# Kernel optimization log

Hardware: AMD Instinct MI355X
Metric: run time of the kernel (lower is better)

The kernel has to match this reference:

```python
import jax, jax.numpy as jnp
import numpy as np

N_P, N_A, N_T = 20000, 10000, 5000
D_IN, D_OUT = 512, 256
E_P, E_A, E_T = 320000, 160000, 80000


def setup_inputs() -> dict:
    key = jax.random.key(0)
    ks = iter(jax.random.split(key, 64))

    def nrm(shape, scale=1.0):
        return jax.random.normal(next(ks), shape, dtype=jnp.float32) * scale

    def xav(shape):
        # xavier_uniform-like scale (gain 1.414), normal draw is fine for a baseline
        return nrm(shape, 1.414 * (2.0 / (shape[0] + shape[1])) ** 0.5)

    def edges(ne, n_src, n_dst):
        src = jax.random.randint(next(ks), (ne,), 0, n_src, dtype=jnp.int32)
        dst = jax.random.randint(next(ks), (ne,), 0, n_dst, dtype=jnp.int32)
        w = jax.random.uniform(next(ks), (ne,), dtype=jnp.float32) / 16.0  # ~normalized adj values
        return src, dst, w

    d = {}
    d["x_p"] = nrm((N_P, D_IN))
    d["x_a"] = nrm((N_A, D_IN))
    d["x_t"] = nrm((N_T, D_IN))
    d["e_p_a_src"], d["e_p_a_dst"], d["e_p_a_w"] = edges(E_P, N_A, N_P)
    d["e_p_t_src"], d["e_p_t_dst"], d["e_p_t_w"] = edges(E_P, N_T, N_P)
    d["e_a_p_src"], d["e_a_p_dst"], d["e_a_p_w"] = edges(E_A, N_P, N_A)
    d["e_a_t_src"], d["e_a_t_dst"], d["e_a_t_w"] = edges(E_A, N_T, N_A)
    d["e_t_p_src"], d["e_t_p_dst"], d["e_t_p_w"] = edges(E_T, N_P, N_T)
    d["e_t_a_src"], d["e_t_a_dst"], d["e_t_a_w"] = edges(E_T, N_A, N_T)
    # parameters for each target type k: W_proj per neighbor, w_self, w_share, w_att, w_cat, bias
    for k, nbs in (("p", ("a", "t")), ("a", ("p", "t")), ("t", ("p", "a"))):
        for nb in nbs:
            d[f"W_{k}_{nb}"] = xav((D_IN, D_OUT))
        d[f"ws_{k}"] = xav((D_IN, D_OUT))
        d[f"wsh_{k}"] = xav((D_OUT, D_OUT))
        d[f"watt_{k}"] = xav((2 * D_OUT, 1))
        d[f"wcat_{k}"] = xav((2 * D_OUT, D_OUT))
        d[f"b_{k}"] = xav((1, D_OUT))
    return d


def _hete_agg(x_self, w_self, w_share, w_att, w_cat, bias, nb_inputs):
    """nb_inputs: list of (x_nb, W_proj, src, dst, edge_w). Faithful to HeteAggregateLayer."""
    n = x_self.shape[0]
    self_ft = (x_self @ w_self) @ w_share  # [n, d]
    # per-relation: project -> spmm (gather + weighted segment-sum over dst) -> share
    nb_fts = [
        jax.ops.segment_sum((x_nb @ Wp)[src] * ew[:, None], dst, num_segments=n) @ w_share
        for (x_nb, Wp, src, dst, ew) in nb_inputs
    ]
    L = len(nb_fts)
    # e = leaky_relu(cat([cat(nb_ft,0), self_ft.repeat(L,1)],1) @ w_att)  -> [L*n, 1]
    e = jnp.concatenate(
        [jax.nn.leaky_relu(jnp.concatenate([f, self_ft], axis=1) @ w_att) for f in nb_fts],
        axis=0,
    )
    # NOTE: faithful replication of the original `e.view(-1, L)` reshape semantics
    att = jax.nn.softmax(e.reshape(n, L), axis=1)  # [n, L]
    agg = nb_fts[0] * att[:, 0:1]
    for i in range(1, L):
        agg = agg + nb_fts[i] * att[:, i : i + 1]
    return jnp.concatenate([agg, self_ft], axis=1) @ w_cat + bias


def reference(x_p, x_a, x_t,
              e_p_a_src, e_p_a_dst, e_p_a_w, e_p_t_src, e_p_t_dst, e_p_t_w,
              e_a_p_src, e_a_p_dst, e_a_p_w, e_a_t_src, e_a_t_dst, e_a_t_w,
              e_t_p_src, e_t_p_dst, e_t_p_w, e_t_a_src, e_t_a_dst, e_t_a_w,
              W_p_a, W_p_t, ws_p, wsh_p, watt_p, wcat_p, b_p,
              W_a_p, W_a_t, ws_a, wsh_a, watt_a, wcat_a, b_a,
              W_t_p, W_t_a, ws_t, wsh_t, watt_t, wcat_t, b_t):
    out_p = _hete_agg(x_p, ws_p, wsh_p, watt_p, wcat_p, b_p,
                      [(x_a, W_p_a, e_p_a_src, e_p_a_dst, e_p_a_w),
                       (x_t, W_p_t, e_p_t_src, e_p_t_dst, e_p_t_w)])
    out_a = _hete_agg(x_a, ws_a, wsh_a, watt_a, wcat_a, b_a,
                      [(x_p, W_a_p, e_a_p_src, e_a_p_dst, e_a_p_w),
                       (x_t, W_a_t, e_a_t_src, e_a_t_dst, e_a_t_w)])
    out_t = _hete_agg(x_t, ws_t, wsh_t, watt_t, wcat_t, b_t,
                      [(x_p, W_t_p, e_t_p_src, e_t_p_dst, e_t_p_w),
                       (x_a, W_t_a, e_t_a_src, e_t_a_dst, e_t_a_w)])
    return (out_p, out_a, out_t)
```

## Files before the change

kernel.cpp:

```cpp
#include <hip/hip_runtime.h>

namespace {

typedef short s16x8 __attribute__((ext_vector_type(8)));
typedef float f32x4 __attribute__((ext_vector_type(4)));

__device__ __forceinline__ float bf2f(unsigned short u) {
  return __uint_as_float(((unsigned)u) << 16);
}
__device__ __forceinline__ unsigned short f2bf(float f) {
  unsigned u = __float_as_uint(f);
  u += 0x7fffu + ((u >> 16) & 1u);
  return (unsigned short)(u >> 16);
}

typedef __attribute__((address_space(3))) unsigned int lds_u32;
typedef __attribute__((address_space(1))) const unsigned int glob_u32;
__device__ __forceinline__ void gl16(const void* g, void* l) {
  __builtin_amdgcn_global_load_lds((glob_u32*)g, (lds_u32*)l, 16, 0, 0);
}

__global__ __launch_bounds__(256) void cvt_x3(const float* __restrict__ x0,
                                              const float* __restrict__ x1,
                                              const float* __restrict__ x2,
                                              unsigned short* __restrict__ out) {
  size_t i = ((size_t)blockIdx.x * 256 + threadIdx.x) * 8;
  const float* src;
  size_t off;
  if (i < (size_t)20000 * 512) { src = x0; off = i; }
  else if (i < (size_t)30000 * 512) { src = x1; off = i - (size_t)20000 * 512; }
  else { src = x2; off = i - (size_t)30000 * 512; }
  float4 a = *(const float4*)(src + off);
  float4 b = *(const float4*)(src + off + 4);
  s16x8 v;
  v[0] = (short)f2bf(a.x); v[1] = (short)f2bf(a.y);
  v[2] = (short)f2bf(a.z); v[3] = (short)f2bf(a.w);
  v[4] = (short)f2bf(b.x); v[5] = (short)f2bf(b.y);
  v[6] = (short)f2bf(b.z); v[7] = (short)f2bf(b.w);
  *(s16x8*)(out + i) = v;
}

struct Tc6 { const float* src[6]; unsigned short* dst[6]; int R[6]; };
__global__ __launch_bounds__(256) void transpose_cvt(Tc6 a) {
  int mat = blockIdx.z;
  int R = a.R[mat];
  int r0 = blockIdx.y * 32, c0 = blockIdx.x * 32;
  if (r0 >= R) return;
  const float* __restrict__ src = a.src[mat];
  unsigned short* __restrict__ dst = a.dst[mat];
  __shared__ float T[32][33];
  int tx = threadIdx.x & 31, ty = threadIdx.x >> 5;
  #pragma unroll
  for (int j = 0; j < 4; ++j) {
    int r = ty + j * 8;
    T[r][tx] = src[(size_t)(r0 + r) * 256 + c0 + tx];
  }
  __syncthreads();
  #pragma unroll
  for (int j = 0; j < 4; ++j) {
    int c = ty + j * 8;
    dst[(size_t)(c0 + c) * R + r0 + tx] = f2bf(T[tx][c]);
  }
}

struct Comb9 { const unsigned short* A[9]; const float* B[9]; unsigned short* C[9]; };
__global__ __launch_bounds__(256) void combine_mfma(Comb9 g) {
  int z = blockIdx.z;
  const unsigned short* __restrict__ A = g.A[z];
  const float* __restrict__ B = g.B[z];
  unsigned short* __restrict__ C = g.C[z];
  int row0 = blockIdx.y * 128;
  int col0 = blockIdx.x * 128;
  __shared__ unsigned short As[128 * 40];
  __shared__ unsigned short Bs[128 * 40];
  int tid = threadIdx.x, lane = tid & 63, w = tid >> 6;
  int quad = lane >> 4, m16 = lane & 15;
  f32x4 acc[2][8];
  #pragma unroll
  for (int r = 0; r < 2; ++r)
    #pragma unroll
    for (int c = 0; c < 8; ++c) acc[r][c] = (f32x4){0.f, 0.f, 0.f, 0.f};
  for (int k0 = 0; k0 < 256; k0 += 32) {
    #pragma unroll
    for (int i = 0; i < 2; ++i) {
      int ch = tid + i * 256;
      int m = ch >> 2, kk = (ch & 3) * 8;
      *(s16x8*)&As[m * 40 + kk] = *(const s16x8*)(A + (size_t)(row0 + m) * 256 + k0 + kk);
      const float4* bp = (const float4*)(B + (size_t)(col0 + m) * 256 + k0 + kk);
      float4 b0 = bp[0], b1 = bp[1];
      s16x8 bv;
      bv[0] = (short)f2bf(b0.x); bv[1] = (short)f2bf(b0.y);
      bv[2] = (short)f2bf(b0.z); bv[3] = (short)f2bf(b0.w);
      bv[4] = (short)f2bf(b1.x); bv[5] = (short)f2bf(b1.y);
      bv[6] = (short)f2bf(b1.z); bv[7] = (short)f2bf(b1.w);
      *(s16x8*)&Bs[m * 40 + kk] = bv;
    }
    __syncthreads();
    s16x8 af[2], bf[8];
    #pragma unroll
    for (int r = 0; r < 2; ++r)
      af[r] = *(const s16x8*)&As[(w * 32 + r * 16 + m16) * 40 + quad * 8];
    #pragma unroll
    for (int c = 0; c < 8; ++c)
      bf[c] = *(const s16x8*)&Bs[(c * 16 + m16) * 40 + quad * 8];
    #pragma unroll
    for (int r = 0; r < 2; ++r)
      #pragma unroll
      for (int c = 0; c < 8; ++c)
        acc[r][c] = __builtin_amdgcn_mfma_f32_16x16x32_bf16(af[r], bf[c], acc[r][c], 0, 0, 0);
    __syncthreads();
  }
  #pragma unroll
  for (int r = 0; r < 2; ++r)
    #pragma unroll
    for (int i = 0; i < 4; ++i) {
      int row = row0 + w * 32 + r * 16 + quad * 4 + i;
      #pragma unroll
      for (int c = 0; c < 8; ++c)
        C[(size_t)row * 512 + col0 + c * 16 + m16] = f2bf(acc[r][c][i]);
    }
}

struct Proj9 { const unsigned short* A[9]; const unsigned short* Bt[9]; unsigned short* C[9]; int M[9]; };
__global__ __launch_bounds__(256) void proj_mfma9(Proj9 g) {
  int z = blockIdx.z;
  int M = g.M[z];
  int row0 = blockIdx.y * 128;
  if (row0 >= M) return;
  int col0 = blockIdx.x * 128;
  const unsigned short* __restrict__ A = g.A[z];
  const unsigned short* __restrict__ Bt = g.Bt[z];
  unsigned short* __restrict__ C = g.C[z];
  __shared__ unsigned short As[128 * 32];
  __shared__ unsigned short Bs[128 * 32];
  int tid = threadIdx.x, lane = tid & 63, w = tid >> 6;
  int quad = lane >> 4, m16 = lane & 15;
  int lr = lane >> 2, lk = (lane & 3) * 8;
  int r0g = row0 + w * 32 + lr;
  int r1g = r0g + 16;
  const unsigned short* a0p = A + (size_t)(r0g < M ? r0g : M - 1) * 512 + lk;
  const unsigned short* a1p = A + (size_t)(r1g < M ? r1g : M - 1) * 512 + lk;
  const unsigned short* b0p = Bt + (size_t)(col0 + w * 32 + lr) * 512 + lk;
  const unsigned short* b1p = b0p + (size_t)16 * 512;
  unsigned short* as0 = &As[w * 1024];
  unsigned short* as1 = &As[w * 1024 + 512];
  unsigned short* bs0 = &Bs[w * 1024];
  unsigned short* bs1 = &Bs[w * 1024 + 512];
  int wr = (w & 1) * 64, wc = (w >> 1) * 64;
  f32x4 acc[4][4];
  #pragma unroll
  for (int r = 0; r < 4; ++r)
    #pragma unroll
    for (int c = 0; c < 4; ++c) acc[r][c] = (f32x4){0.f, 0.f, 0.f, 0.f};
  for (int k0 = 0; k0 < 512; k0 += 32) {
    gl16(a0p + k0, as0);
    gl16(a1p + k0, as1);
    gl16(b0p + k0, bs0);
    gl16(b1p + k0, bs1);
    __syncthreads();
    s16x8 af[4], bf[4];
    #pragma unroll
    for (int r = 0; r < 4; ++r)
      af[r] = *(const s16x8*)&As[(wr + r * 16 + m16) * 32 + quad * 8];
    #pragma unroll
    for (int c = 0; c < 4; ++c)
      bf[c] = *(const s16x8*)&Bs[(wc + c * 16 + m16) * 32 + quad * 8];
    #pragma unroll
    for (int r = 0; r < 4; ++r)
      #pragma unroll
      for (int c = 0; c < 4; ++c)
        acc[r][c] = __builtin_amdgcn_mfma_f32_16x16x32_bf16(af[r], bf[c], acc[r][c], 0, 0, 0);
    __syncthreads();
  }
  #pragma unroll
  for (int r = 0; r < 4; ++r)
    #pragma unroll
    for (int i = 0; i < 4; ++i) {
      int row = row0 + wr + r * 16 + quad * 4 + i;
      if (row < M) {
        #pragma unroll
        for (int c = 0; c < 4; ++c)
          C[(size_t)row * 256 + col0 + wc + c * 16 + m16] = f2bf(acc[r][c][i]);
      }
    }
}

struct Edges6 { const int* src[6]; const int* dst[6]; const float* w[6]; int nE[6]; int cbase[6]; };

#define BSH 9
#define NB2 137
#define CAP2 16384
#define NOV 65536
#define CH 1024
#define NPAY 1120000

__global__ __launch_bounds__(256) void bin1(Edges6 ep,
                                            int* __restrict__ bcur, int* __restrict__ ovcnt,
                                            unsigned long long* __restrict__ rec2,
                                            unsigned long long* __restrict__ ovbuf) {
  int rho = blockIdx.y;
  int nE = ep.nE[rho];
  int chunk = blockIdx.x * CH;
  if (chunk >= nE) return;
  int n = nE - chunk; if (n > CH) n = CH;
  const int* __restrict__ srcp = ep.src[rho];
  const int* __restrict__ dstp = ep.dst[rho];
  const float* __restrict__ wp = ep.w[rho];
  int cb = ep.cbase[rho];
  __shared__ int h[256], excl[256], lcur[256], gbase[256], rsv[256];
  __shared__ int wsum[4];
  __shared__ unsigned long long stage[CH];
  int t = threadIdx.x;
  h[t] = 0;
  gbase[t] = 0;
  __syncthreads();
  int gd[4]; unsigned pv[4];
  #pragma unroll
  for (int j = 0; j < 4; ++j) {
    int idx = t + j * 256;
    gd[j] = -1;
    if (idx < n) {
      int e = chunk + idx;
      int g = cb + dstp[e];
      if (g < 0) g = 0;
      if (g > 69999) g = 69999;
      gd[j] = g;
      pv[j] = (((unsigned)f2bf(wp[e])) << 16) | ((unsigned)srcp[e] & 0x7fffu);
      atomicAdd(&h[g >> BSH], 1);
    }
  }
  __syncthreads();
  int hv = h[t];
  int lane = t & 63, wv = t >> 6;
  int v = hv;
  #pragma unroll
  for (int off = 1; off < 64; off <<= 1) {
    int u = __shfl_up(v, off, 64);
    if (lane >= off) v += u;
  }
  if (lane == 63) wsum[wv] = v;
  __syncthreads();
  int add = 0;
  #pragma unroll
  for (int k = 0; k < 3; ++k)
    if (k < wv) add += wsum[k];
  v += add;
  int ex = v - hv;
  excl[t] = ex;
  lcur[t] = ex;
  int rv = 0;
  if (t < NB2 && hv > 0) {
    rv = (hv + 7) & ~7;
    gbase[t] = atomicAdd(&bcur[t], rv);
  }
  rsv[t] = rv;
  __syncthreads();
  #pragma unroll
  for (int j = 0; j < 4; ++j) {
    if (gd[j] >= 0) {
      int b = gd[j] >> BSH;
      int slot = atomicAdd(&lcur[b], 1);
      if (slot >= 0 && slot < CH)
        stage[slot] = ((unsigned long long)(unsigned)gd[j] << 32) | pv[j];
    }
  }
  __syncthreads();
  for (int s = t; s < n; s += 256) {
    int lo = 0, hi = NB2 - 1;
    while (lo < hi) {
      int mid = (lo + hi + 1) >> 1;
      if (excl[mid] <= s) lo = mid; else hi = mid - 1;
    }
    int b = lo;
    int gp = gbase[b] + (s - excl[b]);
    if (gp >= 0 && gp < CAP2) rec2[(size_t)b * CAP2 + gp] = stage[s];
    else { int op = atomicAdd(ovcnt, 1); ovbuf[op & (NOV - 1)] = stage[s]; }
  }
  for (int b = t; b < NB2; b += 256) {
    int hvb = h[b], rvb = rsv[b], gb = gbase[b];
    for (int k = hvb; k < rvb; ++k) {
      int gp = gb + k;
      if (gp >= 0 && gp < CAP2) rec2[(size_t)b * CAP2 + gp] = 0xFFFFFFFFFFFFFFFFull;
    }
  }
}

__global__ __launch_bounds__(256) void cnt2(const int* __restrict__ bcur,
                                            const unsigned long long* __restrict__ rec2,
                                            const int* __restrict__ ovcnt,
                                            const unsigned long long* __restrict__ ovbuf,
                                            int* __restrict__ counts) {
  int b = blockIdx.x;
  __shared__ int c[512];
  int t = threadIdx.x;
  c[t] = 0; c[t + 256] = 0;
  __syncthreads();
  int nrec = bcur[b];
  nrec = nrec < CAP2 ? nrec : CAP2;
  const unsigned long long* rp = rec2 + (size_t)b * CAP2;
  for (int i = t; i < nrec; i += 256) {
    int gd = (int)(rp[i] >> 32);
    if (gd >= 0) atomicAdd(&c[gd & 511], 1);
  }
  int ovn = *ovcnt;
  ovn = ovn < NOV ? ovn : NOV;
  for (int i = t; i < ovn; i += 256) {
    int gd = (int)(ovbuf[i] >> 32);
    if (gd >= 0 && (gd >> BSH) == b) atomicAdd(&c[gd & 511], 1);
  }
  __syncthreads();
  int g0 = (b << BSH) + t;
  if (g0 < 70000) counts[g0] = c[t];
  int g1 = g0 + 256;
  if (g1 < 70000) counts[g1] = c[t + 256];
}

__global__ __launch_bounds__(256) void scan1(const int* __restrict__ cnt, int* __restrict__ out,
                                             int* __restrict__ part, int len) {
  __shared__ int sh[256];
  int base = blockIdx.x * 2048 + threadIdx.x * 8;
  int v[8];
  int s = 0;
  #pragma unroll
  for (int j = 0; j < 8; ++j) {
    int i = base + j;
    int x = (i < len) ? cnt[i] : 0;
    v[j] = s;
    s += x;
  }
  sh[threadIdx.x] = s;
  __syncthreads();
  for (int off = 1; off < 256; off <<= 1) {
    int t = (threadIdx.x >= off) ? sh[threadIdx.x - off] : 0;
    __syncthreads();
    sh[threadIdx.x] += t;
    __syncthreads();
  }
  int texcl = sh[threadIdx.x] - s;
  #pragma unroll
  for (int j = 0; j < 8; ++j) {
    int i = base + j;
    if (i < len) out[i] = texcl + v[j];
  }
  if (threadIdx.x == 255) part[blockIdx.x] = sh[255];
}

__global__ void scan2(int* __restrict__ part, int nb, int* __restrict__ total_out) {
  __shared__ int sh[64];
  int t = threadIdx.x;
  int v = (t < nb) ? part[t] : 0;
  sh[t] = v;
  __syncthreads();
  for (int off = 1; off < 64; off <<= 1) {
    int x = (t >= off) ? sh[t - off] : 0;
    __syncthreads();
    sh[t] += x;
    __syncthreads();
  }
  if (t < nb) part[t] = sh[t] - v;
  if (t == 63) *total_out = sh[63];
}

__global__ __launch_bounds__(256) void scan3(int* __restrict__ offs,
                                             const int* __restrict__ part, int len) {
  int i = blockIdx.x * 256 + threadIdx.x;
  if (i >= len) return;
  offs[i] += part[i >> 11];
}

__global__ __launch_bounds__(512) void fine2(const int* __restrict__ offs,
                                             const int* __restrict__ bcur,
                                             const unsigned long long* __restrict__ rec2,
                                             const int* __restrict__ ovcnt,
                                             const unsigned long long* __restrict__ ovbuf,
                                             unsigned int* __restrict__ pay) {
  int b = blockIdx.x;
  __shared__ int cur[512];
  int t = threadIdx.x;
  {
    int gd = (b << BSH) + t;
    cur[t] = (gd < 70000) ? offs[gd] : 0;
  }
  __syncthreads();
  int nrec = bcur[b];
  nrec = nrec < CAP2 ? nrec : CAP2;
  const unsigned long long* rp = rec2 + (size_t)b * CAP2;
  for (int i = t; i < nrec; i += 512) {
    unsigned long long r = rp[i];
    int gd = (int)(r >> 32);
    if (gd < 0) continue;
    int pos = atomicAdd(&cur[gd & 511], 1);
    if (pos >= 0 && pos < NPAY) pay[pos] = (unsigned)r;
  }
  int ovn = *ovcnt;
  ovn = ovn < NOV ? ovn : NOV;
  for (int i = t; i < ovn; i += 512) {
    unsigned long long r = ovbuf[i];
    int gd = (int)(r >> 32);
    if (gd >= 0 && (gd >> BSH) == b) {
      int pos = atomicAdd(&cur[gd & 511], 1);
      if (pos >= 0 && pos < NPAY) pay[pos] = (unsigned)r;
    }
  }
}

struct Gather6 { const unsigned short* proj[6]; unsigned short* out[6]; int cb[6]; int n[6]; };
__global__ __launch_bounds__(256) void gather_all(Gather6 g, const int* __restrict__ offs,
                                                  const unsigned int* __restrict__ pay) {
  int rho = blockIdx.y;
  int n = g.n[rho];
  int d = blockIdx.x * 4 + (threadIdx.x >> 6);
  if (d >= n) return;
  int lane = threadIdx.x & 63, half = lane >> 5, l32 = lane & 31;
  const unsigned short* __restrict__ proj = g.proj[rho];
  const int* of = offs + g.cb[rho];
  int s0 = of[d], s1 = of[d + 1];
  float acc[8] = {};
  int e = s0 + half;
  for (; e + 2 < s1; e += 4) {
    unsigned int u0 = pay[e], u1 = pay[e + 2];
    float wt0 = bf2f((unsigned short)(u0 >> 16));
    float wt1 = bf2f((unsigned short)(u1 >> 16));
    s16x8 v0 = *(const s16x8*)(proj + (size_t)(u0 & 0xffffu) * 256 + l32 * 8);
    s16x8 v1 = *(const s16x8*)(proj + (size_t)(u1 & 0xffffu) * 256 + l32 * 8);
    #pragma unroll
    for (int j = 0; j < 8; ++j) {
      acc[j] = fmaf(bf2f((unsigned short)v0[j]), wt0, acc[j]);
      acc[j] = fmaf(bf2f((unsigned short)v1[j]), wt1, acc[j]);
    }
  }
  if (e < s1) {
    unsigned int u = pay[e];
    float wt = bf2f((unsigned short)(u >> 16));
    s16x8 v = *(const s16x8*)(proj + (size_t)(u & 0xffffu) * 256 + l32 * 8);
    #pragma unroll
    for (int j = 0; j < 8; ++j) acc[j] = fmaf(bf2f((unsigned short)v[j]), wt, acc[j]);
  }
  #pragma unroll
  for (int j = 0; j < 8; ++j) acc[j] += __shfl(acc[j], lane ^ 32, 64);
  if (half == 0) {
    s16x8 o;
    #pragma unroll
    for (int j = 0; j < 8; ++j) o[j] = (short)f2bf(acc[j]);
    *(s16x8*)(g.out[rho] + (size_t)d * 256 + l32 * 8) = o;
  }
}

struct Att3 { const unsigned short* nb[3]; const unsigned short* self[3];
              const float* watt[3]; float* att[3]; int n[3]; };
__global__ __launch_bounds__(256) void e_att3(Att3 g) {
  int z = blockIdx.z;
  int n = g.n[z];
  int wv = threadIdx.x >> 6;
  int idx = blockIdx.x * 4 + wv;
  int lane = threadIdx.x & 63;
  __shared__ float ev[4];
  float sum = 0.f;
  if (idx < 2 * n) {
    int i = idx < n ? idx : idx - n;
    ushort4 v  = *(const ushort4*)(g.nb[z] + (size_t)idx * 256 + (lane << 2));
    ushort4 sv = *(const ushort4*)(g.self[z] + (size_t)i * 256 + (lane << 2));
    float4 wa = *(const float4*)(g.watt[z] + (lane << 2));
    float4 wb = *(const float4*)(g.watt[z] + 256 + (lane << 2));
    sum = bf2f(v.x) * wa.x + bf2f(v.y) * wa.y + bf2f(v.z) * wa.z + bf2f(v.w) * wa.w +
          bf2f(sv.x) * wb.x + bf2f(sv.y) * wb.y + bf2f(sv.z) * wb.z + bf2f(sv.w) * wb.w;
    #pragma unroll
    for (int off = 32; off > 0; off >>= 1) sum += __shfl_down(sum, off, 64);
  }
  if (lane == 0) ev[wv] = sum;
  __syncthreads();
  if (threadIdx.x < 2) {
    int base = blockIdx.x * 4 + threadIdx.x * 2;
    if (base < 2 * n) {
      float f0 = ev[threadIdx.x * 2], f1 = ev[threadIdx.x * 2 + 1];
      f0 = f0 > 0.f ? f0 : 0.01f * f0;
      f1 = f1 > 0.f ? f1 : 0.01f * f1;
      float m = fmaxf(f0, f1);
      float a = expf(f0 - m), b = expf(f1 - m);
      float inv = 1.f / (a + b);
      g.att[z][base] = a * inv;
      g.att[z][base + 1] = b * inv;
    }
  }
}

struct Fin3 { const unsigned short* nb[3]; const unsigned short* self[3]; const float* att[3];
              const unsigned short* Wt[3]; const float* bias[3]; float* out[3]; int M[3]; };
__global__ __launch_bounds__(256, 3) void final_mfma3(Fin3 g) {
  int z = blockIdx.z;
  int M = g.M[z];
  int row0 = blockIdx.y * 64;
  if (row0 >= M) return;
  const unsigned short* __restrict__ nbft = g.nb[z];
  const unsigned short* __restrict__ selfb = g.self[z];
  const float* __restrict__ att = g.att[z];
  const unsigned short* __restrict__ Wt = g.Wt[z];
  __shared__ unsigned short As[64 * 40];
  __shared__ unsigned short Bs[256 * 40];
  int tid = threadIdx.x, lane = tid & 63, w = tid >> 6;
  int quad = lane >> 4, m16 = lane & 15;
  int am = tid >> 2, akk = (tid & 3) * 8;
  int gr = row0 + am;
  float a0 = 0.f, a1 = 0.f;
  if (gr < M) { a0 = att[2 * gr]; a1 = att[2 * gr + 1]; }
  f32x4 acc[4][4];
  #pragma unroll
  for (int r = 0; r < 4; ++r)
    #pragma unroll
    for (int c = 0; c < 4; ++c) acc[r][c] = (f32x4){0.f, 0.f, 0.f, 0.f};

  s16x8 pu0 = {}, pu1 = {};
  s16x8 pb[4];

  auto loadA = [&](int k0) {
    int kg = k0 + akk;
    if (gr < M) {
      if (kg < 256) {
        pu0 = *(const s16x8*)(nbft + (size_t)gr * 256 + kg);
        pu1 = *(const s16x8*)(nbft + ((size_t)M + gr) * 256 + kg);
      } else {
        pu0 = *(const s16x8*)(selfb + (size_t)gr * 256 + (kg - 256));
      }
    }
  };
  auto loadB = [&](int k0) {
    #pragma unroll
    for (int i = 0; i < 4; ++i) {
      int ch = tid + i * 256;
      int m = ch >> 2, kk = (ch & 3) * 8;
      pb[i] = *(const s16x8*)(Wt + (size_t)m * 512 + k0 + kk);
    }
  };
  auto storeLDS = [&](int k0) {
    int kg = k0 + akk;
    s16x8 v = {};
    if (gr < M) {
      if (kg < 256) {
        #pragma unroll
        for (int j = 0; j < 8; ++j)
          v[j] = (short)f2bf(fmaf(a0, bf2f((unsigned short)pu0[j]),
                                  a1 * bf2f((unsigned short)pu1[j])));
      } else {
        v = pu0;
      }
    }
    *(s16x8*)&As[am * 40 + akk] = v;
    #pragma unroll
    for (int i = 0; i < 4; ++i) {
      int ch = tid + i * 256;
      int m = ch >> 2, kk = (ch & 3) * 8;
      *(s16x8*)&Bs[m * 40 + kk] = pb[i];
    }
  };

  loadA(0); loadB(0); storeLDS(0);
  __syncthreads();
  for (int k0 = 0; k0 < 512; k0 += 32) {
    int kn = k0 + 32;
    if (kn < 512) { loadA(kn); loadB(kn); }
    s16x8 af[4], bf[4];
    #pragma unroll
    for (int r = 0; r < 4; ++r)
      af[r] = *(const s16x8*)&As[(r * 16 + m16) * 40 + quad * 8];
    #pragma unroll
    for (int c = 0; c < 4; ++c)
      bf[c] = *(const s16x8*)&Bs[(w * 64 + c * 16 + m16) * 40 + quad * 8];
    #pragma unroll
    for (int r = 0; r < 4; ++r)
      #pragma unroll
      for (int c = 0; c < 4; ++c)
        acc[r][c] = __builtin_amdgcn_mfma_f32_16x16x32_bf16(af[r], bf[c], acc[r][c], 0, 0, 0);
    __syncthreads();
    if (kn < 512) {
      storeLDS(kn);
      __syncthreads();
    }
  }
  const float* __restrict__ bias = g.bias[z];
  float* __restrict__ out = g.out[z];
  #pragma unroll
  for (int r = 0; r < 4; ++r)
    #pragma unroll
    for (int i = 0; i < 4; ++i) {
      int row = row0 + r * 16 + quad * 4 + i;
      if (row < M) {
        #pragma unroll
        for (int c = 0; c < 4; ++c) {
          int col = w * 64 + c * 16 + m16;
          out[(size_t)row * 256 + col] = acc[r][c][i] + bias[col];
        }
      }
    }
}

}

extern "C" void kernel_launch(void* const* d_in, const int* in_sizes, int n_in,
                              void* d_out, int out_size, void* d_ws, size_t ws_size,
                              hipStream_t stream) {
  (void)in_sizes; (void)n_in; (void)out_size; (void)ws_size;
  const float* x[3] = {(const float*)d_in[0], (const float*)d_in[1], (const float*)d_in[2]};

  char* p = (char*)d_ws;
  unsigned short* projfull = (unsigned short*)p;  p += (size_t)105000 * 256 * 2;
  unsigned short* nbft = (unsigned short*)p;      p += (size_t)70000 * 256 * 2;
  unsigned short* wcatbt = (unsigned short*)p;    p += (size_t)3 * 256 * 512 * 2;
  int* offs = (int*)p;                            p += (size_t)70004 * 4;
  int* counts = (int*)p;                          p += (size_t)70000 * 4;
  int* bcur = (int*)p;                            p += 160 * 4;
  int* ovcnt = (int*)p;                           p += 16;
  int* part = (int*)p;                            p += 256;
  float* att_buf = (float*)p;                     p += (size_t)70000 * 4;
  unsigned int* csr_pay = (unsigned int*)p;       p += (size_t)1120000 * 4;
  unsigned short* wshT = nbft;
  unsigned short* Wcbt = (unsigned short*)((char*)nbft + 393216);
  unsigned long long* rec2 = (unsigned long long*)projfull;
  unsigned long long* ovbuf = rec2 + (size_t)NB2 * CAP2;
  unsigned short* xb = (unsigned short*)d_out;

  const int n_of[3] = {20000, 10000, 5000};
  const int nbt[3][2] = {{1, 2}, {0, 2}, {0, 1}};
  const int ebase[3][2] = {{3, 6}, {9, 12}, {15, 18}};
  const int nE3[3] = {320000, 160000, 80000};
  const size_t out_off[3] = {0, (size_t)20000 * 256, (size_t)30000 * 256};
  const int tstart[3] = {0, 15000, 40000};
  const int selfoff[3] = {70000, 90000, 100000};
  const int nboff[3] = {0, 40000, 60000};
  const int xboff[3] = {0, 20000, 30000};

  cvt_x3<<<dim3(8750), 256, 0, stream>>>(x[0], x[1], x[2], xb);

  Tc6 tc;
  for (int t = 0; t < 3; ++t) {
    tc.src[t] = (const float*)d_in[21 + t * 7 + 3];
    tc.dst[t] = wshT + (size_t)t * 256 * 256;
    tc.R[t] = 256;
    tc.src[3 + t] = (const float*)d_in[21 + t * 7 + 5];
    tc.dst[3 + t] = wcatbt + (size_t)t * 256 * 512;
    tc.R[3 + t] = 512;
  }
  transpose_cvt<<<dim3(8, 16, 6), 256, 0, stream>>>(tc);

  Comb9 c9;
  for (int t = 0; t < 3; ++t) {
    int wb = 21 + t * 7;
    for (int j = 0; j < 3; ++j) {
      int combo = t * 3 + j;
      c9.A[combo] = wshT + (size_t)t * 256 * 256;
      c9.B[combo] = (const float*)d_in[wb + j];
      c9.C[combo] = Wcbt + (size_t)combo * 256 * 512;
    }
  }
  combine_mfma<<<dim3(4, 2, 9), 256, 0, stream>>>(c9);

  Edges6 ep;
  const int cbase[6] = {0, 20000, 40000, 50000, 60000, 65000};
  for (int t = 0; t < 3; ++t)
    for (int r = 0; r < 2; ++r) {
      int rho = t * 2 + r, eb = ebase[t][r];
      ep.src[rho] = (const int*)d_in[eb];
      ep.dst[rho] = (const int*)d_in[eb + 1];
      ep.w[rho] = (const float*)d_in[eb + 2];
      ep.nE[rho] = nE3[t];
      ep.cbase[rho] = cbase[rho];
    }
  hipMemsetAsync(bcur, 0, 160 * 4 + 16, stream);
  bin1<<<dim3(313, 6), 256, 0, stream>>>(ep, bcur, ovcnt, rec2, ovbuf);
  cnt2<<<NB2, 256, 0, stream>>>(bcur, rec2, ovcnt, ovbuf, counts);
  scan1<<<35, 256, 0, stream>>>(counts, offs, part, 70000);
  scan2<<<1, 64, 0, stream>>>(part, 35, offs + 70000);
  scan3<<<274, 256, 0, stream>>>(offs, part, 70000);
  fine2<<<NB2, 512, 0, stream>>>(offs, bcur, rec2, ovcnt, ovbuf, csr_pay);

  Proj9 pj;
  for (int t = 0; t < 3; ++t) {
    int nb0 = nbt[t][0], nb1 = nbt[t][1];
    int m0 = n_of[nb0];
    pj.A[t * 3 + 0] = xb + (size_t)xboff[nb0] * 512;
    pj.C[t * 3 + 0] = projfull + (size_t)tstart[t] * 256;
    pj.M[t * 3 + 0] = m0;
    pj.A[t * 3 + 1] = xb + (size_t)xboff[nb1] * 512;
    pj.C[t * 3 + 1] = projfull + (size_t)(tstart[t] + m0) * 256;
    pj.M[t * 3 + 1] = n_of[nb1];
    pj.A[t * 3 + 2] = xb + (size_t)xboff[t] * 512;
    pj.C[t * 3 + 2] = projfull + (size_t)selfoff[t] * 256;
    pj.M[t * 3 + 2] = n_of[t];
    for (int j = 0; j < 3; ++j)
      pj.Bt[t * 3 + j] = Wcbt + (size_t)(t * 3 + j) * 256 * 512;
  }
  proj_mfma9<<<dim3(2, 157, 9), 256, 0, stream>>>(pj);

  Gather6 gt;
  for (int t = 0; t < 3; ++t) {
    int m0 = n_of[nbt[t][0]];
    for (int r = 0; r < 2; ++r) {
      int rho = t * 2 + r;
      gt.proj[rho] = projfull + (size_t)(tstart[t] + (r ? m0 : 0)) * 256;
      gt.out[rho] = nbft + (size_t)(nboff[t] + r * n_of[t]) * 256;
      gt.cb[rho] = cbase[rho];
      gt.n[rho] = n_of[t];
    }
  }
  gather_all<<<dim3(5000, 6), 256, 0, stream>>>(gt, offs, csr_pay);

  Att3 at;
  for (int t = 0; t < 3; ++t) {
    at.nb[t] = nbft + (size_t)nboff[t] * 256;
    at.self[t] = projfull + (size_t)selfoff[t] * 256;
    at.watt[t] = (const float*)d_in[21 + t * 7 + 4];
    at.att[t] = att_buf + nboff[t];
    at.n[t] = n_of[t];
  }
  e_att3<<<dim3(10000, 1, 3), 256, 0, stream>>>(at);

  Fin3 fn;
  for (int t = 0; t < 3; ++t) {
    fn.nb[t] = nbft + (size_t)nboff[t] * 256;
    fn.self[t] = projfull + (size_t)selfoff[t] * 256;
    fn.att[t] = att_buf + nboff[t];
    fn.Wt[t] = wcatbt + (size_t)t * 256 * 512;
    fn.bias[t] = (const float*)d_in[21 + t * 7 + 6];
    fn.out[t] = (float*)d_out + out_off[t];
    fn.M[t] = n_of[t];
  }
  final_mfma3<<<dim3(1, 313, 3), 256, 0, stream>>>(fn);
}
```

Before: 406.4 us.

## Regroup projection GEMMs by source node type with full-width tiles and LDS swizzle

The nine projection GEMMs are regrouped by source feature matrix, so each block handles one of three weight combos for a given source type. Each block now computes a full 128x256 output tile instead of 128x128, which halves the number of times A rows are reloaded per weight matrix. An XOR swizzle on the LDS k-offset is added to reduce bank conflicts on fragment reads. The cost is doubled B shared memory and twice as many accumulator registers per thread, which may lower occupancy.

```diff
diff --git a/kernel.cpp b/kernel.cpp
--- a/kernel.cpp
+++ b/kernel.cpp
@@ -121,54 +121,63 @@
     }
 }
 
-struct Proj9 { const unsigned short* A[9]; const unsigned short* Bt[9]; unsigned short* C[9]; int M[9]; };
-__global__ __launch_bounds__(256) void proj_mfma9(Proj9 g) {
-  int z = blockIdx.z;
-  int M = g.M[z];
+struct Proj3 { const unsigned short* A[3]; const unsigned short* Bt[3][3];
+               unsigned short* C[3][3]; int M[3]; };
+__global__ __launch_bounds__(256) void proj_mfma3(Proj3 g) {
+  int s = blockIdx.z;
+  int M = g.M[s];
   int row0 = blockIdx.y * 128;
   if (row0 >= M) return;
-  int col0 = blockIdx.x * 128;
-  const unsigned short* __restrict__ A = g.A[z];
-  const unsigned short* __restrict__ Bt = g.Bt[z];
-  unsigned short* __restrict__ C = g.C[z];
+  int combo = blockIdx.x;
+  const unsigned short* __restrict__ A = g.A[s];
+  const unsigned short* __restrict__ Bt = g.Bt[s][combo];
+  unsigned short* __restrict__ C = g.C[s][combo];
   __shared__ unsigned short As[128 * 32];
-  __shared__ unsigned short Bs[128 * 32];
+  __shared__ unsigned short Bs[256 * 32];
   int tid = threadIdx.x, lane = tid & 63, w = tid >> 6;
   int quad = lane >> 4, m16 = lane & 15;
-  int lr = lane >> 2, lk = (lane & 3) * 8;
-  int r0g = row0 + w * 32 + lr;
-  int r1g = r0g + 16;
-  const unsigned short* a0p = A + (size_t)(r0g < M ? r0g : M - 1) * 512 + lk;
-  const unsigned short* a1p = A + (size_t)(r1g < M ? r1g : M - 1) * 512 + lk;
-  const unsigned short* b0p = Bt + (size_t)(col0 + w * 32 + lr) * 512 + lk;
+  int lr = lane >> 2;
+  int lk = (((lane & 3) ^ (lr & 3) ^ ((lr >> 2) & 3))) * 8;
+  int ar0 = row0 + w * 32 + lr;
+  int ar1 = ar0 + 16;
+  const unsigned short* a0p = A + (size_t)(ar0 < M ? ar0 : M - 1) * 512 + lk;
+  const unsigned short* a1p = A + (size_t)(ar1 < M ? ar1 : M - 1) * 512 + lk;
+  const unsigned short* b0p = Bt + (size_t)(w * 64 + lr) * 512 + lk;
   const unsigned short* b1p = b0p + (size_t)16 * 512;
+  const unsigned short* b2p = b0p + (size_t)32 * 512;
+  const unsigned short* b3p = b0p + (size_t)48 * 512;
   unsigned short* as0 = &As[w * 1024];
   unsigned short* as1 = &As[w * 1024 + 512];
-  unsigned short* bs0 = &Bs[w * 1024];
-  unsigned short* bs1 = &Bs[w * 1024 + 512];
-  int wr = (w & 1) * 64, wc = (w >> 1) * 64;
-  f32x4 acc[4][4];
+  unsigned short* bs0 = &Bs[w * 2048];
+  unsigned short* bs1 = &Bs[w * 2048 + 512];
+  unsigned short* bs2 = &Bs[w * 2048 + 1024];
+  unsigned short* bs3 = &Bs[w * 2048 + 1536];
+  int wr = (w & 1) * 64, wc = (w >> 1) * 128;
+  int sw = ((quad ^ (m16 & 3) ^ ((m16 >> 2) & 3))) * 8;
+  f32x4 acc[4][8];
   #pragma unroll
   for (int r = 0; r < 4; ++r)
     #pragma unroll
-    for (int c = 0; c < 4; ++c) acc[r][c] = (f32x4){0.f, 0.f, 0.f, 0.f};
+    for (int c = 0; c < 8; ++c) acc[r][c] = (f32x4){0.f, 0.f, 0.f, 0.f};
   for (int k0 = 0; k0 < 512; k0 += 32) {
     gl16(a0p + k0, as0);
     gl16(a1p + k0, as1);
     gl16(b0p + k0, bs0);
     gl16(b1p + k0, bs1);
-    __syncthreads();
-    s16x8 af[4], bf[4];
+    gl16(b2p + k0, bs2);
+    gl16(b3p + k0, bs3);
+    __syncthreads();
+    s16x8 af[4], bf[8];
     #pragma unroll
     for (int r = 0; r < 4; ++r)
-      af[r] = *(const s16x8*)&As[(wr + r * 16 + m16) * 32 + quad * 8];
-    #pragma unroll
-    for (int c = 0; c < 4; ++c)
-      bf[c] = *(const s16x8*)&Bs[(wc + c * 16 + m16) * 32 + quad * 8];
+      af[r] = *(const s16x8*)&As[(wr + r * 16 + m16) * 32 + sw];
+    #pragma unroll
+    for (int c = 0; c < 8; ++c)
+      bf[c] = *(const s16x8*)&Bs[(wc + c * 16 + m16) * 32 + sw];
     #pragma unroll
     for (int r = 0; r < 4; ++r)
       #pragma unroll
-      for (int c = 0; c < 4; ++c)
+      for (int c = 0; c < 8; ++c)
         acc[r][c] = __builtin_amdgcn_mfma_f32_16x16x32_bf16(af[r], bf[c], acc[r][c], 0, 0, 0);
     __syncthreads();
   }
@@ -179,8 +188,8 @@
       int row = row0 + wr + r * 16 + quad * 4 + i;
       if (row < M) {
         #pragma unroll
-        for (int c = 0; c < 4; ++c)
-          C[(size_t)row * 256 + col0 + wc + c * 16 + m16] = f2bf(acc[r][c][i]);
+        for (int c = 0; c < 8; ++c)
+          C[(size_t)row * 256 + wc + c * 16 + m16] = f2bf(acc[r][c][i]);
       }
     }
 }
@@ -672,23 +681,28 @@
   scan3<<<274, 256, 0, stream>>>(offs, part, 70000);
   fine2<<<NB2, 512, 0, stream>>>(offs, bcur, rec2, ovcnt, ovbuf, csr_pay);
 
-  Proj9 pj;
-  for (int t = 0; t < 3; ++t) {
-    int nb0 = nbt[t][0], nb1 = nbt[t][1];
-    int m0 = n_of[nb0];
-    pj.A[t * 3 + 0] = xb + (size_t)xboff[nb0] * 512;
-    pj.C[t * 3 + 0] = projfull + (size_t)tstart[t] * 256;
-    pj.M[t * 3 + 0] = m0;
-    pj.A[t * 3 + 1] = xb + (size_t)xboff[nb1] * 512;
-    pj.C[t * 3 + 1] = projfull + (size_t)(tstart[t] + m0) * 256;
-    pj.M[t * 3 + 1] = n_of[nb1];
-    pj.A[t * 3 + 2] = xb + (size_t)xboff[t] * 512;
-    pj.C[t * 3 + 2] = projfull + (size_t)selfoff[t] * 256;
-    pj.M[t * 3 + 2] = n_of[t];
-    for (int j = 0; j < 3; ++j)
-      pj.Bt[t * 3 + j] = Wcbt + (size_t)(t * 3 + j) * 256 * 512;
-  }
-  proj_mfma9<<<dim3(2, 157, 9), 256, 0, stream>>>(pj);
+  Proj3 pj;
+  {
+    int cnum[3] = {0, 0, 0};
+    for (int t = 0; t < 3; ++t) {
+      int m0 = n_of[nbt[t][0]];
+      for (int j = 0; j < 3; ++j) {
+        int s = (j == 2) ? t : nbt[t][j];
+        unsigned short* dst =
+            (j == 0) ? projfull + (size_t)tstart[t] * 256
+          : (j == 1) ? projfull + (size_t)(tstart[t] + m0) * 256
+                     : projfull + (size_t)selfoff[t] * 256;
+        int c = cnum[s]++;
+        pj.Bt[s][c] = Wcbt + (size_t)(t * 3 + j) * 256 * 512;
+        pj.C[s][c] = dst;
+      }
+    }
+    for (int s = 0; s < 3; ++s) {
+      pj.A[s] = xb + (size_t)xboff[s] * 512;
+      pj.M[s] = n_of[s];
+    }
+  }
+  proj_mfma3<<<dim3(3, 157, 3), 256, 0, stream>>>(pj);
 
   Gather6 gt;
   for (int t = 0; t < 3; ++t) {
```

Result: slower. 436.5 us (+7.4%).
